# Kernel tuning notes

Measured on AMD Instinct MI355X. Metric: run time of the kernel, lower is better.

## Reference

```python
import jax, jax.numpy as jnp
import numpy as np

E = 8        # n_experts
H = 1024     # hidden_size == input_size
M = 2048     # intermediate_size
K = 2        # topk
SE = 1       # share_expert
BSZ, SEQ = 2, 1024
W_SCALE = 0.02


def setup_inputs() -> dict:
    key = jax.random.key(0)
    ks = jax.random.split(key, 9)
    return {
        "x": jax.random.normal(ks[0], (BSZ, SEQ, H), jnp.float32),
        "gate_w": jax.random.normal(ks[1], (E, H), jnp.float32) * W_SCALE,
        "beta": jnp.zeros((E,), jnp.float32),
        "gate_proj_w": jax.random.normal(ks[2], (E, H, M), jnp.float32) * W_SCALE,
        "up_proj_w": jax.random.normal(ks[3], (E, H, M), jnp.float32) * W_SCALE,
        "down_proj_w": jax.random.normal(ks[4], (E, M, H), jnp.float32) * W_SCALE,
        "shared_gate_w": jax.random.normal(ks[5], (SE, H, M), jnp.float32) * W_SCALE,
        "shared_up_w": jax.random.normal(ks[6], (SE, H, M), jnp.float32) * W_SCALE,
        "shared_down_w": jax.random.normal(ks[7], (SE, M, H), jnp.float32) * W_SCALE,
    }


def reference(x, gate_w, beta, gate_proj_w, up_proj_w, down_proj_w,
              shared_gate_w, shared_up_w, shared_down_w):
    B0, S0, H0 = x.shape
    xt = x.reshape(-1, H0)                       # [B, H], B = B0*S0 tokens
    B = xt.shape[0]

    # --- routing: top-k on (logits + beta), gate prob = sigmoid(selected logits) ---
    logits = xt @ gate_w.T                       # [B, E]
    _, idx = jax.lax.top_k(logits + beta, K)     # [B, K] expert indices
    probs = jax.nn.sigmoid(jnp.take_along_axis(logits, idx, axis=-1))  # [B, K]

    # combine weights c[b, e]: scatter top-k probs (equivalent to index_add combine)
    c = jnp.zeros((B, E), xt.dtype).at[jnp.arange(B)[:, None], idx].add(probs)

    # --- per-expert SwiGLU over all tokens, then weighted combine by c ---
    g = jnp.einsum('bh,ehm->bem', xt, gate_proj_w)   # [B, E, M]
    u = jnp.einsum('bh,ehm->bem', xt, up_proj_w)     # [B, E, M]
    h = jax.nn.silu(g) * u                           # [B, E, M]
    eo = jnp.einsum('bem,emh->beh', h, down_proj_w)  # [B, E, H]
    combined = jnp.einsum('beh,be->bh', eo, c)       # [B, H]

    # --- shared expert(s): applied to every token, no gating ---
    sg = jnp.einsum('bh,ehm->bem', xt, shared_gate_w)
    su = jnp.einsum('bh,ehm->bem', xt, shared_up_w)
    sh = jax.nn.silu(sg) * su
    shared_out = jnp.einsum('bem,emh->beh', sh, shared_down_w).sum(axis=1)  # [B, H]

    return (combined + shared_out).reshape(B0, S0, H0)
```

## Files before the change

### kernel.cpp

```cpp
#include <hip/hip_runtime.h>

#define NE 8
#define HD 1024
#define MD 2048
#define NT 2048
#define NSH 4224

typedef __attribute__((ext_vector_type(8))) short s16x8;
typedef __attribute__((ext_vector_type(4))) float f32x4;
typedef __attribute__((ext_vector_type(8))) unsigned short u16x8;
typedef __attribute__((ext_vector_type(4))) unsigned short u16x4;

__device__ __forceinline__ unsigned short f2bf(float f) {
    union { float f; unsigned int i; } v; v.f = f;
    unsigned int u = v.i;
    return (unsigned short)((u + 0x7FFFu + ((u >> 16) & 1u)) >> 16);
}
__device__ __forceinline__ float bf2f(unsigned short u) {
    union { unsigned int i; float f; } v; v.i = ((unsigned int)u) << 16; return v.f;
}

__device__ __forceinline__ void gld16(const unsigned short* g, short* l) {
    __builtin_amdgcn_global_load_lds(
        (const __attribute__((address_space(1))) unsigned int*)g,
        (__attribute__((address_space(3))) unsigned int*)l,
        16, 0, 0);
}


__global__ __launch_bounds__(256) void k_cvt_gu(
    const float* __restrict__ wg, const float* __restrict__ wu,
    const float* __restrict__ swg, const float* __restrict__ swu,
    unsigned short* __restrict__ o)
{
    int e = blockIdx.z;
    const float* sg = (e < NE) ? wg + (size_t)e * HD * MD : swg;
    const float* su = (e < NE) ? wu + (size_t)e * HD * MD : swu;
    unsigned short* dst = o + (size_t)e * (2 * MD) * HD;
    int k0 = blockIdx.x * 32, n0 = blockIdx.y * 128;
    __shared__ float T[2 * 32 * 132];
    int tid = threadIdx.x;
    #pragma unroll
    for (int p = 0; p < 4; p++) {
        int idx = p * 256 + tid;
        int row = idx >> 5, l4 = (idx & 31) * 4;
        float4 vg = *(const float4*)(sg + (size_t)(k0 + row) * MD + n0 + l4);
        float4 vu = *(const float4*)(su + (size_t)(k0 + row) * MD + n0 + l4);
        *(float4*)(&T[row * 132 + l4]) = vg;
        *(float4*)(&T[32 * 132 + row * 132 + l4]) = vu;
    }
    __syncthreads();
    const int KC = HD / 8;
    #pragma unroll
    for (int p = 0; p < 4; p++) {
        int c = p * 256 + tid;
        int ni = c & 15, ns = (c >> 4) & 15, kc = c >> 8;
        int colL = ns * 8 + (ni >> 1);
        const float* Tm = &T[(ni & 1) * 32 * 132];
        u16x8 r;
        #pragma unroll
        for (int j = 0; j < 8; j++) r[j] = f2bf(Tm[(kc * 8 + j) * 132 + colL]);
        size_t oidx = ((size_t)((n0 >> 3) + ns) * KC + (k0 >> 3) + kc) * 128 + ni * 8;
        *(u16x8*)(dst + oidx) = r;
    }
}

__global__ __launch_bounds__(256) void k_cvt_d(
    const float* __restrict__ wr, const float* __restrict__ wsd,
    unsigned short* __restrict__ o)
{
    int e = blockIdx.z;
    const float* src = (e < NE) ? wr + (size_t)e * MD * HD : wsd;
    unsigned short* dst = o + (size_t)e * MD * HD;
    int k0 = blockIdx.x * 32, n0 = blockIdx.y * 128;
    __shared__ float T[32 * 132];
    int tid = threadIdx.x;
    #pragma unroll
    for (int p = 0; p < 4; p++) {
        int idx = p * 256 + tid;
        int row = idx >> 5, l4 = (idx & 31) * 4;
        float4 v = *(const float4*)(src + (size_t)(k0 + row) * HD + n0 + l4);
        *(float4*)(&T[row * 132 + l4]) = v;
    }
    __syncthreads();
    const int KC = MD / 8;
    #pragma unroll
    for (int p = 0; p < 2; p++) {
        int c = p * 256 + tid;
        int ni = c & 15, ns = (c >> 4) & 7, kc = c >> 7;
        int colL = ns * 16 + ni;
        u16x8 r;
        #pragma unroll
        for (int j = 0; j < 8; j++) r[j] = f2bf(T[(kc * 8 + j) * 132 + colL]);
        size_t oidx = ((size_t)((n0 >> 4) + ns) * KC + (k0 >> 3) + kc) * 128 + ni * 8;
        *(u16x8*)(dst + oidx) = r;
    }
}

__global__ __launch_bounds__(256) void k_route(
    const float* __restrict__ x, const float* __restrict__ gw,
    const float* __restrict__ beta,
    int* __restrict__ cnt, int* __restrict__ list, int* __restrict__ slot,
    float* __restrict__ rprob, unsigned short* __restrict__ xb)
{
    int wave = threadIdx.x >> 6, lane = threadIdx.x & 63;
    int t = blockIdx.x * 4 + wave;
    const float4* xp = (const float4*)(x + (size_t)t * HD) + lane * 4;
    float4 xv[4];
    #pragma unroll
    for (int j = 0; j < 4; j++) xv[j] = xp[j];

    u16x8 o0, o1;
    o0[0] = f2bf(xv[0].x); o0[1] = f2bf(xv[0].y); o0[2] = f2bf(xv[0].z); o0[3] = f2bf(xv[0].w);
    o0[4] = f2bf(xv[1].x); o0[5] = f2bf(xv[1].y); o0[6] = f2bf(xv[1].z); o0[7] = f2bf(xv[1].w);
    o1[0] = f2bf(xv[2].x); o1[1] = f2bf(xv[2].y); o1[2] = f2bf(xv[2].z); o1[3] = f2bf(xv[2].w);
    o1[4] = f2bf(xv[3].x); o1[5] = f2bf(xv[3].y); o1[6] = f2bf(xv[3].z); o1[7] = f2bf(xv[3].w);
    *(u16x8*)(xb + (size_t)t * HD + lane * 16) = o0;
    *(u16x8*)(xb + (size_t)t * HD + lane * 16 + 8) = o1;

    float logit[NE];
    #pragma unroll
    for (int e = 0; e < NE; e++) {
        const float4* gp = (const float4*)(gw + e * HD) + lane * 4;
        float s = 0.f;
        #pragma unroll
        for (int j = 0; j < 4; j++) {
            float4 g = gp[j];
            s += xv[j].x * g.x + xv[j].y * g.y + xv[j].z * g.z + xv[j].w * g.w;
        }
        for (int off = 32; off > 0; off >>= 1) s += __shfl_xor(s, off);
        logit[e] = s;
    }
    if (lane == 0) {
        float v[NE];
        #pragma unroll
        for (int e = 0; e < NE; e++) v[e] = logit[e] + beta[e];
        int i1 = 0; float m1 = v[0];
        #pragma unroll
        for (int e = 1; e < NE; e++) if (v[e] > m1) { m1 = v[e]; i1 = e; }
        int i2 = -1; float m2 = -3.4e38f;
        #pragma unroll
        for (int e = 0; e < NE; e++) if (e != i1 && v[e] > m2) { m2 = v[e]; i2 = e; }
        if (i2 < 0) i2 = (i1 + 1) & 7;
        float p1 = 1.f / (1.f + __expf(-logit[i1]));
        float p2 = 1.f / (1.f + __expf(-logit[i2]));
        int pos1 = atomicAdd(cnt + i1, 1);
        list[i1 * NT + pos1] = t; slot[t * 2 + 0] = (i1 << 16) | pos1; rprob[t * 2 + 0] = p1;
        int pos2 = atomicAdd(cnt + i2, 1);
        list[i2 * NT + pos2] = t; slot[t * 2 + 1] = (i2 << 16) | pos2; rprob[t * 2 + 1] = p2;
    }
}

__global__ void k_scan(const int* __restrict__ cnt, int* __restrict__ base) {
    if (threadIdx.x == 0) {
        int run = 0;
        for (int e = 0; e < NE; e++) { base[e] = run; run += (cnt[e] + 15) & ~15; }
        base[NE] = run;
    }
}

__global__ __launch_bounds__(256, 4) void k_gateup(
    const unsigned short* __restrict__ x,
    const unsigned short* __restrict__ wgu,
    const int* __restrict__ cnt, const int* __restrict__ base, const int* __restrict__ list,
    unsigned short* __restrict__ h)
{
    int e = blockIdx.z;
    int i0 = blockIdx.y * 128;
    int n0 = blockIdx.x * 128;
    int cnte = (e < NE) ? cnt[e] : NT;
    if (i0 >= cnte) return;
    int rbase = (e < NE) ? base[e] : NSH;
    const unsigned short* wb = wgu + (size_t)e * (2 * MD) * HD;

    __shared__ short As[2][128 * 32];
    __shared__ short Bs[2][8 * 512];
    __shared__ int tok[128];

    int tid = threadIdx.x;
    int lane = tid & 63, wave = tid >> 6;
    if (tid < 128) {
        int gi = i0 + tid;
        tok[tid] = (e < NE) ? ((gi < cnte) ? list[e * NT + gi] : list[e * NT]) : gi;
    }
    __syncthreads();

    int rr = wave * 32 + (lane >> 2);
    int kc = ((lane & 3) ^ ((lane >> 3) & 3)) * 8;
    size_t gaA0 = (size_t)tok[rr] * HD + kc;
    size_t gaA1 = (size_t)tok[rr + 16] * HD + kc;
    const int KC = HD / 8;
    size_t gaB0 = ((size_t)((n0 >> 4) + 2 * wave) * KC) * 128 + lane * 8;
    size_t gaB1 = gaB0 + (size_t)KC * 128;
    int loA0 = (wave * 32) * 32, loA1 = (wave * 32 + 16) * 32;
    int loB0 = (2 * wave) * 512, loB1 = (2 * wave + 1) * 512;

    int wr = (wave >> 1) * 64, wc = (wave & 1) * 64;
    int m = lane & 15, q = lane >> 4;
    int sa = (m >> 1) & 3;

    f32x4 acc[4][4];
    #pragma unroll
    for (int a = 0; a < 4; a++)
        #pragma unroll
        for (int b = 0; b < 4; b++) acc[a][b] = (f32x4)0.f;

    gld16(x + gaA0, &As[0][loA0]);
    gld16(x + gaA1, &As[0][loA1]);
    gld16(wb + gaB0, &Bs[0][loB0]);
    gld16(wb + gaB1, &Bs[0][loB1]);

    int it = 0;
    for (int k0 = 0; k0 < HD; k0 += 32, it ^= 1) {
        __syncthreads();
        int nk = k0 + 32;
        if (nk < HD) {
            int nb = it ^ 1;
            gld16(x + gaA0 + nk, &As[nb][loA0]);
            gld16(x + gaA1 + nk, &As[nb][loA1]);
            gld16(wb + gaB0 + (size_t)nk * 16, &Bs[nb][loB0]);
            gld16(wb + gaB1 + (size_t)nk * 16, &Bs[nb][loB1]);
        }
        s16x8 af[4];
        #pragma unroll
        for (int ti2 = 0; ti2 < 4; ti2++)
            af[ti2] = *(const s16x8*)(&As[it][(wr + ti2 * 16 + m) * 32 + (q ^ sa) * 8]);
        #pragma unroll
        for (int tj = 0; tj < 4; tj++) {
            s16x8 bf = *(const s16x8*)(&Bs[it][((wave & 1) * 4 + tj) * 512 + q * 128 + m * 8]);
            #pragma unroll
            for (int ti2 = 0; ti2 < 4; ti2++)
                acc[ti2][tj] = __builtin_amdgcn_mfma_f32_16x16x32_bf16(af[ti2], bf, acc[ti2][tj], 0, 0, 0);
        }
    }
    #pragma unroll
    for (int ti2 = 0; ti2 < 4; ti2++)
        #pragma unroll
        for (int tj = 0; tj < 4; tj++)
            #pragma unroll
            for (int r = 0; r < 4; r++) {
                float v = acc[ti2][tj][r];
                float uo = __shfl_xor(v, 1);
                int gi = i0 + wr + ti2 * 16 + q * 4 + r;
                if (!(m & 1) && gi < cnte) {
                    float g = v;
                    float hv = (g / (1.f + __expf(-g))) * uo;
                    int col = (n0 + wc + tj * 16 + m) >> 1;
                    int rw = rbase + gi;
                    size_t hi = ((size_t)(rw >> 4) * (MD >> 3) + (col >> 3)) * 128
                              + (rw & 15) * 8 + (col & 7);
                    h[hi] = f2bf(hv);
                }
            }
}

__global__ __launch_bounds__(256, 4) void k_down(
    const unsigned short* __restrict__ wd_all,
    const int* __restrict__ cnt, const int* __restrict__ base,
    const unsigned short* __restrict__ h, unsigned short* __restrict__ eo)
{
    int e = blockIdx.z;
    int i0 = blockIdx.y * 128;
    int n0 = blockIdx.x * 128;
    int cnte = (e < NE) ? cnt[e] : NT;
    if (i0 >= cnte) return;
    int rbase = (e < NE) ? base[e] : NSH;
    const unsigned short* wd = wd_all + (size_t)e * MD * HD;

    __shared__ short As[2][8 * 512];
    __shared__ short Bd[2][8 * 512];

    int tid = threadIdx.x;
    int lane = tid & 63, wave = tid >> 6;
    int r0 = rbase + i0;
    const int KC = MD / 8;
    size_t gaA0 = ((size_t)((r0 >> 4) + 2 * wave) * KC) * 128 + lane * 8;
    size_t gaA1 = gaA0 + (size_t)KC * 128;
    size_t gaB0 = ((size_t)((n0 >> 4) + 2 * wave) * KC) * 128 + lane * 8;
    size_t gaB1 = gaB0 + (size_t)KC * 128;
    int lo0 = (2 * wave) * 512, lo1 = (2 * wave + 1) * 512;

    int wr = (wave >> 1) * 64, wc = (wave & 1) * 64;
    int m = lane & 15, q = lane >> 4;

    f32x4 acc[4][4];
    #pragma unroll
    for (int a = 0; a < 4; a++)
        #pragma unroll
        for (int b = 0; b < 4; b++) acc[a][b] = (f32x4)0.f;

    gld16(h + gaA0, &As[0][lo0]);
    gld16(h + gaA1, &As[0][lo1]);
    gld16(wd + gaB0, &Bd[0][lo0]);
    gld16(wd + gaB1, &Bd[0][lo1]);

    int it = 0;
    for (int k0 = 0; k0 < MD; k0 += 32, it ^= 1) {
        __syncthreads();
        int nk = k0 + 32;
        if (nk < MD) {
            int nb = it ^ 1;
            gld16(h + gaA0 + (size_t)nk * 16, &As[nb][lo0]);
            gld16(h + gaA1 + (size_t)nk * 16, &As[nb][lo1]);
            gld16(wd + gaB0 + (size_t)nk * 16, &Bd[nb][lo0]);
            gld16(wd + gaB1 + (size_t)nk * 16, &Bd[nb][lo1]);
        }
        s16x8 af[4];
        #pragma unroll
        for (int ti2 = 0; ti2 < 4; ti2++)
            af[ti2] = *(const s16x8*)(&As[it][((wave >> 1) * 4 + ti2) * 512 + q * 128 + m * 8]);
        #pragma unroll
        for (int tj = 0; tj < 4; tj++) {
            s16x8 bd = *(const s16x8*)(&Bd[it][((wave & 1) * 4 + tj) * 512 + q * 128 + m * 8]);
            #pragma unroll
            for (int ti2 = 0; ti2 < 4; ti2++)
                acc[ti2][tj] = __builtin_amdgcn_mfma_f32_16x16x32_bf16(af[ti2], bd, acc[ti2][tj], 0, 0, 0);
        }
    }
    #pragma unroll
    for (int ti2 = 0; ti2 < 4; ti2++)
        #pragma unroll
        for (int tj = 0; tj < 4; tj++)
            #pragma unroll
            for (int r = 0; r < 4; r++) {
                int gi = i0 + wr + ti2 * 16 + q * 4 + r;
                if (gi < cnte) {
                    int col = n0 + wc + tj * 16 + m;
                    eo[(size_t)(rbase + gi) * HD + col] = f2bf(acc[ti2][tj][r]);
                }
            }
}

__global__ __launch_bounds__(256) void k_combine(
    const unsigned short* __restrict__ eo, const int* __restrict__ slot,
    const float* __restrict__ rprob, const int* __restrict__ base,
    float* __restrict__ out)
{
    int t = blockIdx.x;
    int s0 = slot[t * 2], s1 = slot[t * 2 + 1];
    float p0 = rprob[t * 2], p1 = rprob[t * 2 + 1];
    int r0 = base[s0 >> 16] + (s0 & 0xFFFF);
    int r1 = base[s1 >> 16] + (s1 & 0xFFFF);
    int rs = NSH + t;
    int c = threadIdx.x * 4;
    u16x4 a = *(const u16x4*)(eo + (size_t)r0 * HD + c);
    u16x4 b = *(const u16x4*)(eo + (size_t)r1 * HD + c);
    u16x4 s = *(const u16x4*)(eo + (size_t)rs * HD + c);
    float4 res;
    res.x = p0 * bf2f(a[0]) + p1 * bf2f(b[0]) + bf2f(s[0]);
    res.y = p0 * bf2f(a[1]) + p1 * bf2f(b[1]) + bf2f(s[1]);
    res.z = p0 * bf2f(a[2]) + p1 * bf2f(b[2]) + bf2f(s[2]);
    res.w = p0 * bf2f(a[3]) + p1 * bf2f(b[3]) + bf2f(s[3]);
    *(float4*)(out + (size_t)t * HD + c) = res;
}

extern "C" void kernel_launch(void* const* d_in, const int* in_sizes, int n_in,
                              void* d_out, int out_size, void* d_ws, size_t ws_size,
                              hipStream_t stream)
{
    const float* x    = (const float*)d_in[0];
    const float* gw   = (const float*)d_in[1];
    const float* beta = (const float*)d_in[2];
    const float* wg   = (const float*)d_in[3];
    const float* wu   = (const float*)d_in[4];
    const float* wd   = (const float*)d_in[5];
    const float* swg  = (const float*)d_in[6];
    const float* swu  = (const float*)d_in[7];
    const float* swd  = (const float*)d_in[8];
    float* out = (float*)d_out;

    char* ws = (char*)d_ws;
    const size_t MB = (size_t)1 << 20;
    int*   cnt   = (int*)(ws + 0);
    int*   basep = (int*)(ws + 64);
    int*   list  = (int*)(ws + 1024);
    int*   slot  = (int*)(ws + 1024 + 65536);
    float* rprob = (float*)(ws + 1024 + 65536 + 16384);
    unsigned short* xb   = (unsigned short*)(ws + 1 * MB);
    unsigned short* eo   = (unsigned short*)(ws + 6 * MB);
    unsigned short* wgut = (unsigned short*)(ws + 20 * MB);
    unsigned short* wdt  = (unsigned short*)(ws + 92 * MB);
    unsigned short* h    = (unsigned short*)(ws + 128 * MB);

    hipMemsetAsync(ws, 0, 128, stream);

    dim3 tgu(HD / 32, MD / 128, NE + 1);
    k_cvt_gu<<<tgu, 256, 0, stream>>>(wg, wu, swg, swu, wgut);
    dim3 td(MD / 32, HD / 128, NE + 1);
    k_cvt_d<<<td, 256, 0, stream>>>(wd, swd, wdt);

    k_route<<<NT / 4, 256, 0, stream>>>(x, gw, beta, cnt, list, slot, rprob, xb);
    k_scan<<<1, 64, 0, stream>>>(cnt, basep);

    dim3 g3(2 * MD / 128, NT / 128, NE + 1);
    k_gateup<<<g3, 256, 0, stream>>>(xb, wgut, cnt, basep, list, h);

    dim3 g4(HD / 128, NT / 128, NE + 1);
    k_down<<<g4, 256, 0, stream>>>(wdt, cnt, basep, h, eo);

    k_combine<<<NT, 256, 0, stream>>>(eo, slot, rprob, basep, out);
}
```

Measured before the change: 440.0 us.

## Merge weight conversion kernels, use packed bf16 convert, drop scan kernel

Replaces the two LDS-transposing weight conversion kernels with one kernel in which each thread reads a column strided over K and emits packed bf16 via v_cvt_pk_bf16_f32, writing the same tiled layouts. Removes the k_scan launch by recomputing each expert's padded base offset from the counts inside the gate/up, down and combine kernels. The aim is fewer launches and cheaper conversion, but the new conversion uses only 192x9 blocks with a serial 16-step loop per thread and column-strided global reads, which may lower bandwidth.

```diff
diff --git a/kernel.cpp b/kernel.cpp
--- a/kernel.cpp
+++ b/kernel.cpp
@@ -19,6 +19,11 @@
 __device__ __forceinline__ float bf2f(unsigned short u) {
     union { unsigned int i; float f; } v; v.i = ((unsigned int)u) << 16; return v.f;
 }
+__device__ __forceinline__ unsigned int cvtpk(float lo, float hi) {
+    unsigned int r;
+    asm volatile("v_cvt_pk_bf16_f32 %0, %1, %2" : "=v"(r) : "v"(lo), "v"(hi));
+    return r;
+}
 
 __device__ __forceinline__ void gld16(const unsigned short* g, short* l) {
     __builtin_amdgcn_global_load_lds(
@@ -27,73 +32,55 @@
         16, 0, 0);
 }
 
-
-__global__ __launch_bounds__(256) void k_cvt_gu(
+__device__ __forceinline__ int padbase(const int* __restrict__ cnt, int e) {
+    int run = 0;
+    for (int ee = 0; ee < e; ee++) run += (cnt[ee] + 15) & ~15;
+    return run;
+}
+
+
+__global__ __launch_bounds__(256) void k_cvt_w(
     const float* __restrict__ wg, const float* __restrict__ wu,
     const float* __restrict__ swg, const float* __restrict__ swu,
-    unsigned short* __restrict__ o)
-{
-    int e = blockIdx.z;
-    const float* sg = (e < NE) ? wg + (size_t)e * HD * MD : swg;
-    const float* su = (e < NE) ? wu + (size_t)e * HD * MD : swu;
-    unsigned short* dst = o + (size_t)e * (2 * MD) * HD;
-    int k0 = blockIdx.x * 32, n0 = blockIdx.y * 128;
-    __shared__ float T[2 * 32 * 132];
+    const float* __restrict__ wd, const float* __restrict__ swd,
+    unsigned short* __restrict__ ogu, unsigned short* __restrict__ od)
+{
+    int b = blockIdx.x, e = blockIdx.y;
     int tid = threadIdx.x;
-    #pragma unroll
-    for (int p = 0; p < 4; p++) {
-        int idx = p * 256 + tid;
-        int row = idx >> 5, l4 = (idx & 31) * 4;
-        float4 vg = *(const float4*)(sg + (size_t)(k0 + row) * MD + n0 + l4);
-        float4 vu = *(const float4*)(su + (size_t)(k0 + row) * MD + n0 + l4);
-        *(float4*)(&T[row * 132 + l4]) = vg;
-        *(float4*)(&T[32 * 132 + row * 132 + l4]) = vu;
-    }
-    __syncthreads();
-    const int KC = HD / 8;
-    #pragma unroll
-    for (int p = 0; p < 4; p++) {
-        int c = p * 256 + tid;
-        int ni = c & 15, ns = (c >> 4) & 15, kc = c >> 8;
-        int colL = ns * 8 + (ni >> 1);
-        const float* Tm = &T[(ni & 1) * 32 * 132];
-        u16x8 r;
-        #pragma unroll
-        for (int j = 0; j < 8; j++) r[j] = f2bf(Tm[(kc * 8 + j) * 132 + colL]);
-        size_t oidx = ((size_t)((n0 >> 3) + ns) * KC + (k0 >> 3) + kc) * 128 + ni * 8;
-        *(u16x8*)(dst + oidx) = r;
-    }
-}
-
-__global__ __launch_bounds__(256) void k_cvt_d(
-    const float* __restrict__ wr, const float* __restrict__ wsd,
-    unsigned short* __restrict__ o)
-{
-    int e = blockIdx.z;
-    const float* src = (e < NE) ? wr + (size_t)e * MD * HD : wsd;
-    unsigned short* dst = o + (size_t)e * MD * HD;
-    int k0 = blockIdx.x * 32, n0 = blockIdx.y * 128;
-    __shared__ float T[32 * 132];
-    int tid = threadIdx.x;
-    #pragma unroll
-    for (int p = 0; p < 4; p++) {
-        int idx = p * 256 + tid;
-        int row = idx >> 5, l4 = (idx & 31) * 4;
-        float4 v = *(const float4*)(src + (size_t)(k0 + row) * HD + n0 + l4);
-        *(float4*)(&T[row * 132 + l4]) = v;
-    }
-    __syncthreads();
-    const int KC = MD / 8;
-    #pragma unroll
-    for (int p = 0; p < 2; p++) {
-        int c = p * 256 + tid;
-        int ni = c & 15, ns = (c >> 4) & 7, kc = c >> 7;
-        int colL = ns * 16 + ni;
-        u16x8 r;
-        #pragma unroll
-        for (int j = 0; j < 8; j++) r[j] = f2bf(T[(kc * 8 + j) * 132 + colL]);
-        size_t oidx = ((size_t)((n0 >> 4) + ns) * KC + (k0 >> 3) + kc) * 128 + ni * 8;
-        *(u16x8*)(dst + oidx) = r;
+    if (b < 128) {
+        int nb = b & 15, kb = b >> 4;
+        int ni = nb * 256 + tid;
+        const float* sg = (e < NE) ? wg + (size_t)e * HD * MD : swg;
+        const float* su = (e < NE) ? wu + (size_t)e * HD * MD : swu;
+        const float* s = (ni & 1) ? su : sg;
+        int n = ni >> 1;
+        unsigned short* dst = ogu + (size_t)e * (2 * MD) * HD
+                            + (size_t)(ni >> 4) * 128 * 128 + (ni & 15) * 8;
+        for (int kc = kb * 16; kc < kb * 16 + 16; kc++) {
+            float v[8];
+            #pragma unroll
+            for (int j = 0; j < 8; j++) v[j] = s[(size_t)(kc * 8 + j) * MD + n];
+            uint4 r;
+            r.x = cvtpk(v[0], v[1]); r.y = cvtpk(v[2], v[3]);
+            r.z = cvtpk(v[4], v[5]); r.w = cvtpk(v[6], v[7]);
+            *(uint4*)(dst + (size_t)kc * 128) = r;
+        }
+    } else {
+        int b2 = b - 128;
+        int nb = b2 & 3, kb = b2 >> 2;
+        int ni = nb * 256 + tid;
+        const float* s = (e < NE) ? wd + (size_t)e * MD * HD : swd;
+        unsigned short* dst = od + (size_t)e * MD * HD
+                            + (size_t)(ni >> 4) * 256 * 128 + (ni & 15) * 8;
+        for (int kc = kb * 16; kc < kb * 16 + 16; kc++) {
+            float v[8];
+            #pragma unroll
+            for (int j = 0; j < 8; j++) v[j] = s[(size_t)(kc * 8 + j) * HD + ni];
+            uint4 r;
+            r.x = cvtpk(v[0], v[1]); r.y = cvtpk(v[2], v[3]);
+            r.z = cvtpk(v[4], v[5]); r.w = cvtpk(v[6], v[7]);
+            *(uint4*)(dst + (size_t)kc * 128) = r;
+        }
     }
 }
 
@@ -151,18 +138,10 @@
     }
 }
 
-__global__ void k_scan(const int* __restrict__ cnt, int* __restrict__ base) {
-    if (threadIdx.x == 0) {
-        int run = 0;
-        for (int e = 0; e < NE; e++) { base[e] = run; run += (cnt[e] + 15) & ~15; }
-        base[NE] = run;
-    }
-}
-
 __global__ __launch_bounds__(256, 4) void k_gateup(
     const unsigned short* __restrict__ x,
     const unsigned short* __restrict__ wgu,
-    const int* __restrict__ cnt, const int* __restrict__ base, const int* __restrict__ list,
+    const int* __restrict__ cnt, const int* __restrict__ list,
     unsigned short* __restrict__ h)
 {
     int e = blockIdx.z;
@@ -170,7 +149,7 @@
     int n0 = blockIdx.x * 128;
     int cnte = (e < NE) ? cnt[e] : NT;
     if (i0 >= cnte) return;
-    int rbase = (e < NE) ? base[e] : NSH;
+    int rbase = (e < NE) ? padbase(cnt, e) : NSH;
     const unsigned short* wb = wgu + (size_t)e * (2 * MD) * HD;
 
     __shared__ short As[2][128 * 32];
@@ -256,7 +235,7 @@
 
 __global__ __launch_bounds__(256, 4) void k_down(
     const unsigned short* __restrict__ wd_all,
-    const int* __restrict__ cnt, const int* __restrict__ base,
+    const int* __restrict__ cnt,
     const unsigned short* __restrict__ h, unsigned short* __restrict__ eo)
 {
     int e = blockIdx.z;
@@ -264,7 +243,7 @@
     int n0 = blockIdx.x * 128;
     int cnte = (e < NE) ? cnt[e] : NT;
     if (i0 >= cnte) return;
-    int rbase = (e < NE) ? base[e] : NSH;
+    int rbase = (e < NE) ? padbase(cnt, e) : NSH;
     const unsigned short* wd = wd_all + (size_t)e * MD * HD;
 
     __shared__ short As[2][8 * 512];
@@ -333,14 +312,21 @@
 
 __global__ __launch_bounds__(256) void k_combine(
     const unsigned short* __restrict__ eo, const int* __restrict__ slot,
-    const float* __restrict__ rprob, const int* __restrict__ base,
+    const float* __restrict__ rprob, const int* __restrict__ cnt,
     float* __restrict__ out)
 {
     int t = blockIdx.x;
     int s0 = slot[t * 2], s1 = slot[t * 2 + 1];
     float p0 = rprob[t * 2], p1 = rprob[t * 2 + 1];
-    int r0 = base[s0 >> 16] + (s0 & 0xFFFF);
-    int r1 = base[s1 >> 16] + (s1 & 0xFFFF);
+    int e0 = s0 >> 16, e1 = s1 >> 16;
+    int run = 0, b0 = 0, b1 = 0;
+    for (int ee = 0; ee < NE; ee++) {
+        if (ee == e0) b0 = run;
+        if (ee == e1) b1 = run;
+        run += (cnt[ee] + 15) & ~15;
+    }
+    int r0 = b0 + (s0 & 0xFFFF);
+    int r1 = b1 + (s1 & 0xFFFF);
     int rs = NSH + t;
     int c = threadIdx.x * 4;
     u16x4 a = *(const u16x4*)(eo + (size_t)r0 * HD + c);
@@ -372,7 +358,6 @@
     char* ws = (char*)d_ws;
     const size_t MB = (size_t)1 << 20;
     int*   cnt   = (int*)(ws + 0);
-    int*   basep = (int*)(ws + 64);
     int*   list  = (int*)(ws + 1024);
     int*   slot  = (int*)(ws + 1024 + 65536);
     float* rprob = (float*)(ws + 1024 + 65536 + 16384);
@@ -384,19 +369,16 @@
 
     hipMemsetAsync(ws, 0, 128, stream);
 
-    dim3 tgu(HD / 32, MD / 128, NE + 1);
-    k_cvt_gu<<<tgu, 256, 0, stream>>>(wg, wu, swg, swu, wgut);
-    dim3 td(MD / 32, HD / 128, NE + 1);
-    k_cvt_d<<<td, 256, 0, stream>>>(wd, swd, wdt);
+    dim3 gc(192, NE + 1);
+    k_cvt_w<<<gc, 256, 0, stream>>>(wg, wu, swg, swu, wd, swd, wgut, wdt);
 
     k_route<<<NT / 4, 256, 0, stream>>>(x, gw, beta, cnt, list, slot, rprob, xb);
-    k_scan<<<1, 64, 0, stream>>>(cnt, basep);
 
     dim3 g3(2 * MD / 128, NT / 128, NE + 1);
-    k_gateup<<<g3, 256, 0, stream>>>(xb, wgut, cnt, basep, list, h);
+    k_gateup<<<g3, 256, 0, stream>>>(xb, wgut, cnt, list, h);
 
     dim3 g4(HD / 128, NT / 128, NE + 1);
-    k_down<<<g4, 256, 0, stream>>>(wdt, cnt, basep, h, eo);
-
-    k_combine<<<NT, 256, 0, stream>>>(eo, slot, rprob, basep, out);
-}
+    k_down<<<g4, 256, 0, stream>>>(wdt, cnt, h, eo);
+
+    k_combine<<<NT, 256, 0, stream>>>(eo, slot, rprob, cnt, out);
+}
```

After: 449.2 us. 2.1% more time.
